# Kernel tuning notes

Measured on AMD Instinct MI355X. Metric: run time of the kernel, lower is better.

The kernel has to match this reference:

```python
import jax, jax.numpy as jnp
import numpy as np
from jax.scipy.linalg import expm

D = 512      # d_model
S = 3        # num_scales
BATCH = 256
H = 8        # attention heads
HD = D // H  # head dim


def layernorm(x, g, b, eps=1e-5):
    m = jnp.mean(x, axis=-1, keepdims=True)
    v = jnp.var(x, axis=-1, keepdims=True)
    return (x - m) / jnp.sqrt(v + eps) * g + b


def setup_inputs() -> dict:
    key = jax.random.key(0)
    ks = jax.random.split(key, 16)
    sd = 1.0 / np.sqrt(D)
    inp = {
        'x': jax.random.normal(ks[0], (BATCH, D), jnp.float32),
        'h_prev': jax.random.normal(ks[1], (BATCH, D), jnp.float32),
        'lstm_h': jax.random.normal(ks[2], (S, BATCH, D), jnp.float32) * 0.1,
        'lstm_c': jax.random.normal(ks[3], (S, BATCH, D), jnp.float32) * 0.1,
        'A': jax.random.normal(ks[4], (D, D), jnp.float32) * sd,
        'Bm': jax.random.normal(ks[5], (D, D), jnp.float32) * sd,
        'dn_w1': jax.random.normal(ks[6], (D, D), jnp.float32) * sd,
        'dn_b1': jnp.zeros((D,), jnp.float32),
        'dn_g': jnp.ones((D,), jnp.float32),
        'dn_beta': jnp.zeros((D,), jnp.float32),
        'dn_w2': jax.random.normal(ks[7], (1, D), jnp.float32) * sd,
        'dn_b2': jnp.zeros((1,), jnp.float32),
        'lstm_wih': jax.random.normal(ks[8], (S, 4 * D, D), jnp.float32) * sd,
        'lstm_whh': jax.random.normal(ks[9], (S, 4 * D, D), jnp.float32) * sd,
        'lstm_bih': jnp.zeros((S, 4 * D), jnp.float32),
        'lstm_bhh': jnp.zeros((S, 4 * D), jnp.float32),
        'decays': jnp.linspace(0.5, 0.95, S, dtype=jnp.float32),
        'attn_in_w': jax.random.normal(ks[10], (3 * D, D), jnp.float32) * sd,
        'attn_in_b': jnp.zeros((3 * D,), jnp.float32),
        'attn_out_w': jax.random.normal(ks[11], (D, D), jnp.float32) * sd,
        'attn_out_b': jnp.zeros((D,), jnp.float32),
        'proj_w': jax.random.normal(ks[12], (D, (S + 2) * D), jnp.float32) * (1.0 / np.sqrt((S + 2) * D)),
        'proj_b': jnp.zeros((D,), jnp.float32),
        'proj_g': jnp.ones((D,), jnp.float32),
        'proj_beta': jnp.zeros((D,), jnp.float32),
    }
    return inp


def reference(x, h_prev, lstm_h, lstm_c, A, Bm, dn_w1, dn_b1, dn_g, dn_beta,
              dn_w2, dn_b2, lstm_wih, lstm_whh, lstm_bih, lstm_bhh, decays,
              attn_in_w, attn_in_b, attn_out_w, attn_out_b,
              proj_w, proj_b, proj_g, proj_beta):
    # ---- delta_net: Linear -> LayerNorm -> GELU(exact) -> Linear -> Softplus ----
    h1 = layernorm(x @ dn_w1.T + dn_b1, dn_g, dn_beta)
    h1 = jax.nn.gelu(h1, approximate=False)
    delta = jax.nn.softplus(h1 @ dn_w2.T + dn_b2)           # (B, 1)

    # ---- SSM update: h_t = expm(delta*A) h_prev + delta*B x ----
    A_disc = jax.vmap(expm)(delta[:, :, None] * A)          # (B, D, D)
    h_ssm = jnp.einsum('bij,bj->bi', A_disc, h_prev) + delta * jnp.einsum('ij,bj->bi', Bm, x)

    # ---- multi-scale LSTM cells (vectorized over scales) ----
    gates = (jnp.einsum('bd,skd->sbk', x, lstm_wih)
             + jnp.einsum('sbd,skd->sbk', lstm_h, lstm_whh)
             + (lstm_bih + lstm_bhh)[:, None, :])           # (S, B, 4D)
    gi, gf, gg, go = jnp.split(gates, 4, axis=-1)
    i_g = jax.nn.sigmoid(gi)
    f_g = jax.nn.sigmoid(gf)
    g_g = jnp.tanh(gg)
    o_g = jax.nn.sigmoid(go)
    c_raw = f_g * lstm_c + i_g * g_g                        # (S, B, D)
    h_new = o_g * jnp.tanh(c_raw)                           # (S, B, D)
    dec = decays[:, None, None]
    c_new = dec * lstm_c + (1.0 - dec) * c_raw              # (S, B, D)

    # ---- fusion attention: 1 query (h_ssm), S keys/values (h_new) ----
    Wq, Wk, Wv = jnp.split(attn_in_w, 3, axis=0)
    bq, bk, bv = jnp.split(attn_in_b, 3, axis=0)
    kv = jnp.transpose(h_new, (1, 0, 2))                    # (B, S, D)
    q = (h_ssm @ Wq.T + bq).reshape(-1, 1, H, HD).transpose(0, 2, 1, 3)   # (B,H,1,HD)
    k = (kv @ Wk.T + bk).reshape(-1, S, H, HD).transpose(0, 2, 1, 3)      # (B,H,S,HD)
    v = (kv @ Wv.T + bv).reshape(-1, S, H, HD).transpose(0, 2, 1, 3)
    scores = jnp.einsum('bhqe,bhke->bhqk', q, k) / np.sqrt(HD)
    attn = jax.nn.softmax(scores, axis=-1)
    ctx = jnp.einsum('bhqk,bhke->bhqe', attn, v)            # (B,H,1,HD)
    ctx = ctx.transpose(0, 2, 1, 3).reshape(-1, D)          # (B, D)
    fused = ctx @ attn_out_w.T + attn_out_b                 # (B, D)

    # ---- output projection over concat [h_ssm, fused, h_1..h_S] ----
    combined = jnp.concatenate([h_ssm, fused] + [h_new[i] for i in range(S)], axis=-1)
    output = layernorm(combined @ proj_w.T + proj_b, proj_g, proj_beta)
    return (output, h_ssm, h_new, c_new)
```

## Files before the change

### kernel.cpp

```cpp
#include <hip/hip_runtime.h>
#include <math.h>

#define DIM 512
#define NB 256
#define KMAX 12

using bf16x8 = __attribute__((ext_vector_type(8))) short;
using f32x4  = __attribute__((ext_vector_type(4))) float;
using float4v = __attribute__((ext_vector_type(4))) float;
using ushort4v = __attribute__((ext_vector_type(4))) unsigned short;

__device__ __forceinline__ unsigned short f2b(float f) {
    union { float f; unsigned int u; } v; v.f = f;
    unsigned int r = v.u + 0x7fffu + ((v.u >> 16) & 1u);
    return (unsigned short)(r >> 16);
}
__device__ __forceinline__ float b2f(unsigned short u) {
    union { unsigned int u; float f; } v; v.u = ((unsigned int)u) << 16;
    return v.f;
}
__device__ __forceinline__ ushort4v f2b4(float4v v) {
    ushort4v o;
    o.x = f2b(v.x); o.y = f2b(v.y); o.z = f2b(v.z); o.w = f2b(v.w);
    return o;
}

__device__ __forceinline__ void block_reduce2(float& s, float& q, float* sb1, float* sb2)
{
    int tid = threadIdx.x;
    #pragma unroll
    for (int off = 32; off > 0; off >>= 1) {
        s += __shfl_down(s, off);
        q += __shfl_down(q, off);
    }
    if ((tid & 63) == 0) { sb1[tid >> 6] = s; sb2[tid >> 6] = q; }
    __syncthreads();
    s = sb1[0] + sb1[1] + sb1[2] + sb1[3];
    q = sb2[0] + sb2[1] + sb2[2] + sb2[3];
    __syncthreads();
}

struct GemmDesc {
    const unsigned short* X;
    const unsigned short* W;
    const float* bias;
    float* Cf;
    unsigned short* Cb;
    unsigned short* Ct;
    int M, N, K, ldX, ldW, ldC, tr_row0, acc;
};
struct GemmArgs { GemmDesc d[8]; };
struct LnParams {
    const float* pre; const float* g; const float* beta;
    const float* w2; const float* b2; float* delta; float* coeff;
    int lnd_y;
    const float* cin; const float* bih; const float* bhh; const float* decays;
    float* hout; float* cout; unsigned short* combb;
};

__global__ __launch_bounds__(256) void gemm_mfma(GemmArgs args, LnParams lp)
{
    __shared__ unsigned short lsA[2][8192];
    __shared__ unsigned short lsB[2][8192];
    __shared__ float sb1[4], sb2[4];

    if ((int)blockIdx.y == lp.lnd_y) {
        int b = blockIdx.x, tid = threadIdx.x;
        int i0 = tid, i1 = tid + 256;
        float x0 = lp.pre[(size_t)b * DIM + i0];
        float x1 = lp.pre[(size_t)b * DIM + i1];
        float s = x0 + x1, q = x0 * x0 + x1 * x1;
        block_reduce2(s, q, sb1, sb2);
        float mean = s * (1.f / DIM);
        float var  = q * (1.f / DIM) - mean * mean;
        float inv  = rsqrtf(var + 1e-5f);
        float y0 = (x0 - mean) * inv * lp.g[i0] + lp.beta[i0];
        float y1 = (x1 - mean) * inv * lp.g[i1] + lp.beta[i1];
        float h0 = 0.5f * y0 * (1.f + erff(y0 * 0.70710678118654752f));
        float h1 = 0.5f * y1 * (1.f + erff(y1 * 0.70710678118654752f));
        float p = h0 * lp.w2[i0] + h1 * lp.w2[i1];
        float dummy = 0.f;
        block_reduce2(p, dummy, sb1, sb2);
        if (tid == 0) {
            float z = p + lp.b2[0];
            float d = (z > 20.f) ? z : log1pf(expf(z));
            lp.delta[b] = d;
            float c = 1.f;
            lp.coeff[b] = 1.f;
            for (int k = 1; k <= KMAX; ++k) { c *= d / (float)k; lp.coeff[k * 256 + b] = c; }
        }
        return;
    }

    GemmDesc de = args.d[blockIdx.y];
    int tmm = de.M >> 6;
    int tiles = tmm * (de.N >> 6);
    int t = blockIdx.x;
    if (t >= tiles) return;
    int qc = tiles >> 3, rc = tiles & 7;
    int xcd = t & 7, li = t >> 3;
    int tt = (xcd < rc) ? (xcd * (qc + 1) + li) : (rc * (qc + 1) + (xcd - rc) * qc + li);
    int m0 = (tt % tmm) << 6;
    int n0 = (tt / tmm) << 6;

    int tid = threadIdx.x;
    int w = tid >> 6;
    int l = tid & 63;
    int nkt = de.K >> 7;

    int srow = w * 16 + (l >> 2);
    int schk = l & 3;
    const unsigned short* gA = de.X + (size_t)(m0 + srow) * de.ldX + schk * 8;
    const unsigned short* gB = de.W + (size_t)(n0 + srow) * de.ldW + schk * 8;
    unsigned short* lA = &lsA[0][(w * 64 + l) * 8];
    unsigned short* lB = &lsB[0][(w * 64 + l) * 8];

#define STAGE(bufi, kt)                                                          \
    do {                                                                         \
        for (int hh = 0; hh < 4; ++hh) {                                         \
            __builtin_amdgcn_global_load_lds(                                    \
                (const __attribute__((address_space(1))) unsigned int*)(gA + (size_t)(kt) * 128 + hh * 32), \
                (__attribute__((address_space(3))) unsigned int*)(lA + (bufi) * 8192 + hh * 2048), 16, 0, 0); \
            __builtin_amdgcn_global_load_lds(                                    \
                (const __attribute__((address_space(1))) unsigned int*)(gB + (size_t)(kt) * 128 + hh * 32), \
                (__attribute__((address_space(3))) unsigned int*)(lB + (bufi) * 8192 + hh * 2048), 16, 0, 0); \
        }                                                                        \
    } while (0)

    int mbase = (w >> 1) * 32;
    int nbase = (w & 1) * 32;

    f32x4 acc[2][2];
    #pragma unroll
    for (int i = 0; i < 2; ++i)
        #pragma unroll
        for (int j = 0; j < 2; ++j)
            acc[i][j] = (f32x4){0.f, 0.f, 0.f, 0.f};

    int kg = l >> 4;
    int fr = l & 15;
    int aslot = (mbase * 4 + fr * 4 + kg) * 8;
    int bslot = (nbase * 4 + fr * 4 + kg) * 8;

    STAGE(0, 0);

    for (int kt = 0; kt < nkt; ++kt) {
        __syncthreads();
        if (kt + 1 < nkt) STAGE((kt + 1) & 1, kt + 1);

        const unsigned short* bufA = &lsA[kt & 1][0];
        const unsigned short* bufB = &lsB[kt & 1][0];
        #pragma unroll
        for (int h = 0; h < 4; ++h) {
            bf16x8 a0 = *(const bf16x8*)(bufA + h * 2048 + aslot);
            bf16x8 a1 = *(const bf16x8*)(bufA + h * 2048 + aslot + 512);
            bf16x8 b0 = *(const bf16x8*)(bufB + h * 2048 + bslot);
            bf16x8 b1 = *(const bf16x8*)(bufB + h * 2048 + bslot + 512);
            acc[0][0] = __builtin_amdgcn_mfma_f32_16x16x32_bf16(a0, b0, acc[0][0], 0, 0, 0);
            acc[0][1] = __builtin_amdgcn_mfma_f32_16x16x32_bf16(a0, b1, acc[0][1], 0, 0, 0);
            acc[1][0] = __builtin_amdgcn_mfma_f32_16x16x32_bf16(a1, b0, acc[1][0], 0, 0, 0);
            acc[1][1] = __builtin_amdgcn_mfma_f32_16x16x32_bf16(a1, b1, acc[1][1], 0, 0, 0);
        }
    }

    if (de.acc == 3) {
        __syncthreads();
        float* tile = (float*)lsA;
        #pragma unroll
        for (int mi = 0; mi < 2; ++mi)
            #pragma unroll
            for (int ni = 0; ni < 2; ++ni) {
                int ct = nbase + ni * 16 + fr;
                #pragma unroll
                for (int r = 0; r < 4; ++r) {
                    int rt = mbase + mi * 16 + kg * 4 + r;
                    tile[rt * 65 + ct] = acc[mi][ni][r];
                }
            }
        __syncthreads();
        int s = de.tr_row0;
        int d0 = n0 >> 2;
        float dec = lp.decays[s];
        for (int cell = tid; cell < 1024; cell += 256) {
            int row = cell >> 4, dsub = cell & 15;
            int d = d0 + dsub;
            int b = m0 + row;
            float vgi = tile[row * 65 +      dsub] + lp.bih[s * 2048 +        d] + lp.bhh[s * 2048 +        d];
            float vgf = tile[row * 65 + 16 + dsub] + lp.bih[s * 2048 +  512 + d] + lp.bhh[s * 2048 +  512 + d];
            float vgg = tile[row * 65 + 32 + dsub] + lp.bih[s * 2048 + 1024 + d] + lp.bhh[s * 2048 + 1024 + d];
            float vgo = tile[row * 65 + 48 + dsub] + lp.bih[s * 2048 + 1536 + d] + lp.bhh[s * 2048 + 1536 + d];
            float cc = lp.cin[(size_t)s * 131072 + (size_t)b * 512 + d];
            float ig = 1.f / (1.f + expf(-vgi));
            float fg = 1.f / (1.f + expf(-vgf));
            float g_ = tanhf(vgg);
            float og = 1.f / (1.f + expf(-vgo));
            float craw = fg * cc + ig * g_;
            float hn = og * tanhf(craw);
            lp.hout[(size_t)s * 131072 + (size_t)b * 512 + d] = hn;
            lp.cout[(size_t)s * 131072 + (size_t)b * 512 + d] = dec * cc + (1.f - dec) * craw;
            lp.combb[(size_t)b * 2048 + 512 + s * 512 + d] = f2b(hn);
        }
        return;
    }

    #pragma unroll
    for (int mi = 0; mi < 2; ++mi) {
        #pragma unroll
        for (int ni = 0; ni < 2; ++ni) {
            int col = n0 + nbase + ni * 16 + fr;
            float bv = de.bias ? de.bias[col] : 0.f;
            #pragma unroll
            for (int r = 0; r < 4; ++r) {
                int row = m0 + mbase + mi * 16 + (l >> 4) * 4 + r;
                float v = acc[mi][ni][r] + bv;
                if (de.Cf) {
                    if (de.acc == 2)      atomicAdd(&de.Cf[(size_t)row * de.ldC + col], v);
                    else if (de.acc == 1) de.Cf[(size_t)row * de.ldC + col] += v;
                    else                  de.Cf[(size_t)row * de.ldC + col] = v;
                } else {
                    de.Cb[(size_t)row * de.ldC + col] = f2b(v);
                }
                if (de.Ct && row >= de.tr_row0)
                    de.Ct[(size_t)col * 512 + (row - de.tr_row0)] = f2b(v);
            }
        }
    }
#undef STAGE
}

#define NSEG 13
struct PrepArgs {
    const float* sA[NSEG]; const float* sB[NSEG]; unsigned short* dst[NSEG];
    int n4[NSEG], dRL4[NSEG], sRLA4[NSEG], sRLB4[NSEG], half4[NSEG], offA[NSEG], gmap[NSEG];
    const float* A; unsigned short* ATb;
    const float* W2src; unsigned short* W2dst;
    const float* projw; const float* projb; const float* aoutb; float* pbc;
};
__global__ __launch_bounds__(256) void prep_kernel(PrepArgs a)
{
    __shared__ float tile[32][33];
    int bid = blockIdx.x, tid = threadIdx.x;
    if (bid < 2048) {
        const int gstride = 2048 * 256;
        int g0 = bid * 256 + tid;
        for (int seg = 0; seg < NSEG; ++seg) {
            int n4 = a.n4[seg];
            const float* sA = a.sA[seg];
            const float* sB = a.sB[seg];
            unsigned short* d = a.dst[seg];
            int dRL4 = a.dRL4[seg], sRLA4 = a.sRLA4[seg], sRLB4 = a.sRLB4[seg];
            int half4 = a.half4[seg], offA = a.offA[seg], gm = a.gmap[seg];
            for (int i = g0; i < n4; i += gstride) {
                int r = i / dRL4, c = i - r * dRL4;
                int rs = gm ? (((r >> 4) & 3) * 512 + ((r >> 6) << 4) + (r & 15)) : r;
                const float* src = (c < half4)
                    ? sA + ((size_t)rs * sRLA4 + offA + c) * 4
                    : sB + ((size_t)rs * sRLB4 + (c - half4)) * 4;
                float4v v = *(const float4v*)src;
                *(ushort4v*)(d + (size_t)i * 4) = f2b4(v);
            }
        }
    } else if (bid < 2560) {
        int tt = bid - 2048;
        const float* src = a.A;
        unsigned short* dst = a.ATb;
        if (tt >= 256) { tt -= 256; src = a.W2src; dst = a.W2dst; }
        int bx = tt & 15, by = tt >> 4;
        int tx = tid & 31, ty = tid >> 5;
        #pragma unroll
        for (int i = 0; i < 32; i += 8)
            tile[ty + i][tx] = src[(size_t)(by * 32 + ty + i) * 512 + bx * 32 + tx];
        __syncthreads();
        #pragma unroll
        for (int i = 0; i < 32; i += 8)
            dst[(size_t)(bx * 32 + ty + i) * 512 + by * 32 + tx] = f2b(tile[tx][ty + i]);
    } else {
        int i = (bid - 2560) * 256 + tid;
        const float* pr = a.projw + (size_t)i * 2560 + 512;
        float acc = 0.f;
        for (int j = 0; j < 512; j += 4) {
            float4v w = *(const float4v*)(pr + j);
            float4v ab = *(const float4v*)(a.aoutb + j);
            acc += w.x * ab.x + w.y * ab.y + w.z * ab.z + w.w * ab.w;
        }
        a.pbc[i] = a.projb[i] + acc;
    }
}

__global__ void pointwise_fused(
    const float* __restrict__ Tm, const float* __restrict__ coeff,
    const float* __restrict__ h_prev, const float* __restrict__ delta,
    const float* __restrict__ Bx, float* __restrict__ hssm,
    unsigned short* __restrict__ combb)
{
    int idx4 = blockIdx.x * 256 + threadIdx.x;
    int base = idx4 * 4;
    int b = base >> 9, i = base & 511;
    const float* Tr = Tm + (size_t)b * (KMAX * DIM) + i;
    float4v a = *(const float4v*)(h_prev + base);
    #pragma unroll
    for (int k = 1; k <= KMAX; ++k) {
        float c = coeff[k * 256 + b];
        float4v t = *(const float4v*)(Tr + (size_t)(k - 1) * DIM);
        a.x += c * t.x; a.y += c * t.y; a.z += c * t.z; a.w += c * t.w;
    }
    float dl = delta[b];
    float4v bx = *(const float4v*)(Bx + base);
    a.x += dl * bx.x; a.y += dl * bx.y; a.z += dl * bx.z; a.w += dl * bx.w;
    *(float4v*)(hssm + base) = a;
    *(ushort4v*)(combb + (size_t)b * 2048 + i) = f2b4(a);
}

__global__ __launch_bounds__(256) void tail_kernel(
    const unsigned short* __restrict__ qb, const unsigned short* __restrict__ kvb,
    const unsigned short* __restrict__ M2b, const float* __restrict__ projA,
    const float* __restrict__ fin_g, const float* __restrict__ fin_beta,
    float* __restrict__ outp)
{
    __shared__ float ctxs[512];
    __shared__ float sb1[4], sb2[4];
    int b = blockIdx.x, tid = threadIdx.x;

    if (tid < 128) {
        int h = tid >> 4, sub = (tid & 15) * 4;
        int col = h * 64 + sub;
        ushort4v q4 = *(const ushort4v*)(qb + (size_t)b * 512 + col);
        float qf[4] = { b2f(q4.x), b2f(q4.y), b2f(q4.z), b2f(q4.w) };
        float p[3];
        ushort4v k4[3], v4[3];
        #pragma unroll
        for (int s = 0; s < 3; ++s) {
            k4[s] = *(const ushort4v*)(kvb + (size_t)s * 262144 + (size_t)b * 1024 + col);
            v4[s] = *(const ushort4v*)(kvb + (size_t)s * 262144 + (size_t)b * 1024 + 512 + col);
            p[s] = qf[0] * b2f(k4[s].x) + qf[1] * b2f(k4[s].y)
                 + qf[2] * b2f(k4[s].z) + qf[3] * b2f(k4[s].w);
        }
        #pragma unroll
        for (int off = 1; off < 16; off <<= 1) {
            p[0] += __shfl_xor(p[0], off);
            p[1] += __shfl_xor(p[1], off);
            p[2] += __shfl_xor(p[2], off);
        }
        const float scale = 0.125f;
        float p0 = p[0] * scale, p1 = p[1] * scale, p2 = p[2] * scale;
        float m = fmaxf(p0, fmaxf(p1, p2));
        float w0 = expf(p0 - m), w1 = expf(p1 - m), w2 = expf(p2 - m);
        float invs = 1.f / (w0 + w1 + w2);
        ctxs[col + 0] = (w0 * b2f(v4[0].x) + w1 * b2f(v4[1].x) + w2 * b2f(v4[2].x)) * invs;
        ctxs[col + 1] = (w0 * b2f(v4[0].y) + w1 * b2f(v4[1].y) + w2 * b2f(v4[2].y)) * invs;
        ctxs[col + 2] = (w0 * b2f(v4[0].z) + w1 * b2f(v4[1].z) + w2 * b2f(v4[2].z)) * invs;
        ctxs[col + 3] = (w0 * b2f(v4[0].w) + w1 * b2f(v4[1].w) + w2 * b2f(v4[2].w)) * invs;
    }
    __syncthreads();

    float x0 = projA[(size_t)b * 512 + tid];
    float x1 = projA[(size_t)b * 512 + tid + 256];
    {
        const unsigned short* mr0 = M2b + (size_t)tid * 512;
        const unsigned short* mr1 = M2b + (size_t)(tid + 256) * 512;
        for (int k = 0; k < 512; k += 8) {
            ushort4v a0 = *(const ushort4v*)(mr0 + k);
            ushort4v a1 = *(const ushort4v*)(mr0 + k + 4);
            ushort4v c0 = *(const ushort4v*)(mr1 + k);
            ushort4v c1 = *(const ushort4v*)(mr1 + k + 4);
            float t0 = ctxs[k+0], t1 = ctxs[k+1], t2 = ctxs[k+2], t3 = ctxs[k+3];
            float t4 = ctxs[k+4], t5 = ctxs[k+5], t6 = ctxs[k+6], t7 = ctxs[k+7];
            x0 += t0*b2f(a0.x) + t1*b2f(a0.y) + t2*b2f(a0.z) + t3*b2f(a0.w)
                + t4*b2f(a1.x) + t5*b2f(a1.y) + t6*b2f(a1.z) + t7*b2f(a1.w);
            x1 += t0*b2f(c0.x) + t1*b2f(c0.y) + t2*b2f(c0.z) + t3*b2f(c0.w)
                + t4*b2f(c1.x) + t5*b2f(c1.y) + t6*b2f(c1.z) + t7*b2f(c1.w);
        }
    }

    float s = x0 + x1, q = x0 * x0 + x1 * x1;
    block_reduce2(s, q, sb1, sb2);
    float mean = s * (1.f / DIM);
    float var  = q * (1.f / DIM) - mean * mean;
    float inv  = rsqrtf(var + 1e-5f);
    outp[(size_t)b * DIM + tid]       = (x0 - mean) * inv * fin_g[tid]       + fin_beta[tid];
    outp[(size_t)b * DIM + tid + 256] = (x1 - mean) * inv * fin_g[tid + 256] + fin_beta[tid + 256];
}

extern "C" void kernel_launch(void* const* d_in, const int* in_sizes, int n_in,
                              void* d_out, int out_size, void* d_ws, size_t ws_size,
                              hipStream_t stream)
{
    const float* x        = (const float*)d_in[0];
    const float* h_prev   = (const float*)d_in[1];
    const float* lstm_h   = (const float*)d_in[2];
    const float* lstm_c   = (const float*)d_in[3];
    const float* A        = (const float*)d_in[4];
    const float* Bm       = (const float*)d_in[5];
    const float* dn_w1    = (const float*)d_in[6];
    const float* dn_b1    = (const float*)d_in[7];
    const float* dn_g     = (const float*)d_in[8];
    const float* dn_beta  = (const float*)d_in[9];
    const float* dn_w2    = (const float*)d_in[10];
    const float* dn_b2    = (const float*)d_in[11];
    const float* wih      = (const float*)d_in[12];
    const float* whh      = (const float*)d_in[13];
    const float* bih      = (const float*)d_in[14];
    const float* bhh      = (const float*)d_in[15];
    const float* decays   = (const float*)d_in[16];
    const float* ain_w    = (const float*)d_in[17];
    const float* ain_b    = (const float*)d_in[18];
    const float* aout_w   = (const float*)d_in[19];
    const float* aout_b   = (const float*)d_in[20];
    const float* proj_w   = (const float*)d_in[21];
    const float* proj_b   = (const float*)d_in[22];
    const float* proj_g   = (const float*)d_in[23];
    const float* proj_bt  = (const float*)d_in[24];

    float* out  = (float*)d_out;
    float* hssm = out + 131072;
    float* hnew = out + 262144;
    float* cnew = out + 655360;

    unsigned short* us = (unsigned short*)d_ws;
    unsigned short* hpb     = us;
    unsigned short* ATb     = us + 131072;
    unsigned short* dn_w1b  = us + 393216;
    unsigned short* Bmb     = us + 655360;
    unsigned short* ain_wb  = us + 917504;
    unsigned short* proj_wb = us + 1703936;
    unsigned short* P2b     = us + 2752512;
    unsigned short* aout_wTb= us + 3014656;
    unsigned short* Pw      = us + 3276800;
    unsigned short* Qa      = us + 5373952;
    unsigned short* Qb      = us + 5636096;
    unsigned short* Wcat    = us + 5898240;
    unsigned short* Xcat    = us + 12189696;
    unsigned short* combb   = us + 12976128;
    unsigned short* qb      = us + 13500416;
    unsigned short* kvb     = us + 13631488;
    unsigned short* U8b     = us + 14417920;
    float* fbase  = (float*)(us + 14548992);
    float* pre1   = fbase;
    float* delta  = fbase + 131072;
    float* coeff  = fbase + 131328;
    float* Bx     = fbase + 134656;
    float* Tm     = fbase + 265728;
    float* pbc    = fbase + 1838592;
    unsigned short* M2b = (unsigned short*)(fbase + 1839616);
    float* projout = pre1;

    LnParams lpOff;
    lpOff.pre = nullptr; lpOff.g = nullptr; lpOff.beta = nullptr;
    lpOff.w2 = nullptr; lpOff.b2 = nullptr; lpOff.delta = nullptr; lpOff.coeff = nullptr;
    lpOff.lnd_y = -1;
    lpOff.cin = lstm_c; lpOff.bih = bih; lpOff.bhh = bhh; lpOff.decays = decays;
    lpOff.hout = hnew; lpOff.cout = cnew; lpOff.combb = combb;

    PrepArgs pa;
    int sidx = 0;
    auto LIN = [&](const float* s, unsigned short* d, int n4) {
        pa.sA[sidx]=s; pa.sB[sidx]=s; pa.dst[sidx]=d; pa.n4[sidx]=n4;
        pa.dRL4[sidx]=n4; pa.sRLA4[sidx]=0; pa.sRLB4[sidx]=0;
        pa.half4[sidx]=n4; pa.offA[sidx]=0; pa.gmap[sidx]=0; ++sidx;
    };
    LIN(h_prev, hpb,     32768);
    LIN(A,      Pw,      65536);
    LIN(dn_w1,  dn_w1b,  65536);
    LIN(Bm,     Bmb,     65536);
    LIN(ain_w,  ain_wb,  196608);
    pa.sA[sidx]=proj_w; pa.sB[sidx]=proj_w + 1024; pa.dst[sidx]=proj_wb; pa.n4[sidx]=262144;
    pa.dRL4[sidx]=512; pa.sRLA4[sidx]=640; pa.sRLB4[sidx]=640; pa.half4[sidx]=128; pa.offA[sidx]=0; pa.gmap[sidx]=0; ++sidx;
    pa.sA[sidx]=proj_w; pa.sB[sidx]=proj_w; pa.dst[sidx]=P2b; pa.n4[sidx]=65536;
    pa.dRL4[sidx]=128; pa.sRLA4[sidx]=640; pa.sRLB4[sidx]=640; pa.half4[sidx]=128; pa.offA[sidx]=128; pa.gmap[sidx]=0; ++sidx;
    for (int s = 0; s < 3; ++s) {
        pa.sA[sidx]=wih + (size_t)s*1048576; pa.sB[sidx]=whh + (size_t)s*1048576;
        pa.dst[sidx]=Wcat + (size_t)s*2097152; pa.n4[sidx]=524288;
        pa.dRL4[sidx]=256; pa.sRLA4[sidx]=128; pa.sRLB4[sidx]=128; pa.half4[sidx]=128; pa.offA[sidx]=0;
        pa.gmap[sidx]=1; ++sidx;
    }
    for (int s = 0; s < 3; ++s) {
        pa.sA[sidx]=x; pa.sB[sidx]=lstm_h + (size_t)s*131072;
        pa.dst[sidx]=Xcat + (size_t)s*262144; pa.n4[sidx]=65536;
        pa.dRL4[sidx]=256; pa.sRLA4[sidx]=128; pa.sRLB4[sidx]=128; pa.half4[sidx]=128; pa.offA[sidx]=0;
        pa.gmap[sidx]=0; ++sidx;
    }
    pa.A = A; pa.ATb = ATb;
    pa.W2src = aout_w; pa.W2dst = aout_wTb;
    pa.projw = proj_w; pa.projb = proj_b; pa.aoutb = aout_b; pa.pbc = pbc;
    prep_kernel<<<2562, 256, 0, stream>>>(pa);

    GemmArgs ga;
    ga.d[0] = { Xcat, dn_w1b, dn_b1, pre1, nullptr, nullptr, 256, 512, 512, 1024, 512, 512, 0, 0 };
    ga.d[1] = { Xcat, Bmb,    nullptr, Bx,  nullptr, nullptr, 256, 512, 512, 1024, 512, 512, 0, 0 };
    ga.d[2] = { Pw, ATb, nullptr, nullptr, Pw + 1*262144, Qa, 512, 512, 512, 512, 512, 512, 0, 0 };
    for (int s = 0; s < 3; ++s)
        ga.d[3 + s] = { Xcat + (size_t)s * 262144, Wcat + (size_t)s * 2097152, nullptr,
                        nullptr, nullptr, nullptr,
                        256, 2048, 1024, 1024, 1024, 2048, s, 3 };
    ga.d[6] = { P2b, aout_wTb, nullptr, nullptr, M2b, nullptr, 512, 512, 512, 512, 512, 512, 0, 0 };
    gemm_mfma<<<dim3(128, 7), 256, 0, stream>>>(ga, lpOff);

    LnParams lp1 = lpOff;
    lp1.pre = pre1; lp1.g = dn_g; lp1.beta = dn_beta; lp1.w2 = dn_w2; lp1.b2 = dn_b2;
    lp1.delta = delta; lp1.coeff = coeff; lp1.lnd_y = 1;
    ga.d[0] = { Pw, Qa, nullptr, nullptr, Pw + 2*262144, Qb, 1024, 512, 512, 512, 512, 512, 512, 0 };
    gemm_mfma<<<dim3(256, 2), 256, 0, stream>>>(ga, lp1);

    ga.d[0] = { Pw, Qb, nullptr, nullptr, Pw + 4*262144, nullptr, 2048, 512, 512, 512, 512, 512, 0, 0 };
    gemm_mfma<<<dim3(256, 1), 256, 0, stream>>>(ga, lpOff);

    ga.d[0] = { hpb, Pw, nullptr, Tm, nullptr, nullptr, 256, 4096, 512, 512, 512, 6144, 0, 0 };
    ga.d[1] = { hpb, Pw + 7*262144, nullptr, nullptr, U8b, nullptr, 256, 512, 512, 512, 512, 512, 0, 0 };
    gemm_mfma<<<dim3(256, 2), 256, 0, stream>>>(ga, lpOff);

    ga.d[0] = { U8b, Pw, nullptr, Tm + 4096, nullptr, nullptr, 256, 2048, 512, 512, 512, 6144, 0, 0 };
    gemm_mfma<<<dim3(128, 1), 256, 0, stream>>>(ga, lpOff);

    pointwise_fused<<<128, 256, 0, stream>>>(Tm, coeff, h_prev, delta, Bx, hssm, combb);

    ga.d[0] = { combb, ain_wb, ain_b, nullptr, qb, nullptr, 256, 512, 512, 2048, 512, 512, 0, 0 };
    for (int s = 0; s < 3; ++s)
        ga.d[1 + s] = { combb + 512 + (size_t)s * 512, ain_wb + 262144, ain_b + 512,
                        nullptr, kvb + (size_t)s * 262144, nullptr, 256, 1024, 512, 2048, 512, 1024, 0, 0 };
    ga.d[4] = { combb, proj_wb, pbc, projout, nullptr, nullptr, 256, 512, 2048, 2048, 2048, 512, 0, 0 };
    gemm_mfma<<<dim3(64, 5), 256, 0, stream>>>(ga, lpOff);

    tail_kernel<<<256, 256, 0, stream>>>(qb, kvb, M2b, projout,
                                         proj_g, proj_bt, out);
}
```

Before: 233.4 us.

## Interleave Taylor-series power products with matrix-power squaring chain

```diff
diff --git a/kernel.cpp b/kernel.cpp
--- a/kernel.cpp
+++ b/kernel.cpp
@@ -47,7 +47,7 @@
     float* Cf;
     unsigned short* Cb;
     unsigned short* Ct;
-    int M, N, K, ldX, ldW, ldC, tr_row0, acc;
+    int M, N, K, ldX, ldW, ldC, ldCb, tr_row0, acc;
 };
 struct GemmArgs { GemmDesc d[8]; };
 struct LnParams {
@@ -217,9 +217,9 @@
                     if (de.acc == 2)      atomicAdd(&de.Cf[(size_t)row * de.ldC + col], v);
                     else if (de.acc == 1) de.Cf[(size_t)row * de.ldC + col] += v;
                     else                  de.Cf[(size_t)row * de.ldC + col] = v;
-                } else {
-                    de.Cb[(size_t)row * de.ldC + col] = f2b(v);
                 }
+                if (de.Cb)
+                    de.Cb[(size_t)row * de.ldCb + col] = f2b(v);
                 if (de.Ct && row >= de.tr_row0)
                     de.Ct[(size_t)col * 512 + (row - de.tr_row0)] = f2b(v);
             }
@@ -433,15 +433,15 @@
     unsigned short* combb   = us + 12976128;
     unsigned short* qb      = us + 13500416;
     unsigned short* kvb     = us + 13631488;
-    unsigned short* U8b     = us + 14417920;
-    float* fbase  = (float*)(us + 14548992);
+    unsigned short* Tmb     = us + 14417920;
+    float* fbase  = (float*)(us + 14942208);
     float* pre1   = fbase;
     float* delta  = fbase + 131072;
     float* coeff  = fbase + 131328;
     float* Bx     = fbase + 134656;
     float* Tm     = fbase + 265728;
     float* pbc    = fbase + 1838592;
-    unsigned short* M2b = (unsigned short*)(fbase + 1839616);
+    unsigned short* M2b = (unsigned short*)(fbase + 1839104);
     float* projout = pre1;
 
     LnParams lpOff;
@@ -485,39 +485,46 @@
     prep_kernel<<<2562, 256, 0, stream>>>(pa);
 
     GemmArgs ga;
-    ga.d[0] = { Xcat, dn_w1b, dn_b1, pre1, nullptr, nullptr, 256, 512, 512, 1024, 512, 512, 0, 0 };
-    ga.d[1] = { Xcat, Bmb,    nullptr, Bx,  nullptr, nullptr, 256, 512, 512, 1024, 512, 512, 0, 0 };
-    ga.d[2] = { Pw, ATb, nullptr, nullptr, Pw + 1*262144, Qa, 512, 512, 512, 512, 512, 512, 0, 0 };
+    ga.d[0] = { Xcat, dn_w1b, dn_b1, pre1, nullptr, nullptr, 256, 512, 512, 1024, 512, 512, 0, 0, 0 };
+    ga.d[1] = { Xcat, Bmb,    nullptr, Bx,  nullptr, nullptr, 256, 512, 512, 1024, 512, 512, 0, 0, 0 };
+    ga.d[2] = { Pw, ATb, nullptr, nullptr, Pw + 1*262144, Qa, 512, 512, 512, 512, 512, 512, 512, 0, 0 };
     for (int s = 0; s < 3; ++s)
         ga.d[3 + s] = { Xcat + (size_t)s * 262144, Wcat + (size_t)s * 2097152, nullptr,
                         nullptr, nullptr, nullptr,
-                        256, 2048, 1024, 1024, 1024, 2048, s, 3 };
-    ga.d[6] = { P2b, aout_wTb, nullptr, nullptr, M2b, nullptr, 512, 512, 512, 512, 512, 512, 0, 0 };
-    gemm_mfma<<<dim3(128, 7), 256, 0, stream>>>(ga, lpOff);
+                        256, 2048, 1024, 1024, 1024, 2048, 0, s, 3 };
+    ga.d[6] = { P2b, aout_wTb, nullptr, nullptr, M2b, nullptr, 512, 512, 512, 512, 512, 512, 512, 0, 0 };
+    ga.d[7] = { hpb, Pw, nullptr, Tm, Tmb, nullptr, 256, 512, 512, 512, 512, 6144, 2048, 0, 0 };
+    gemm_mfma<<<dim3(128, 8), 256, 0, stream>>>(ga, lpOff);
 
     LnParams lp1 = lpOff;
     lp1.pre = pre1; lp1.g = dn_g; lp1.beta = dn_beta; lp1.w2 = dn_w2; lp1.b2 = dn_b2;
-    lp1.delta = delta; lp1.coeff = coeff; lp1.lnd_y = 1;
-    ga.d[0] = { Pw, Qa, nullptr, nullptr, Pw + 2*262144, Qb, 1024, 512, 512, 512, 512, 512, 512, 0 };
-    gemm_mfma<<<dim3(256, 2), 256, 0, stream>>>(ga, lp1);
-
-    ga.d[0] = { Pw, Qb, nullptr, nullptr, Pw + 4*262144, nullptr, 2048, 512, 512, 512, 512, 512, 0, 0 };
-    gemm_mfma<<<dim3(256, 1), 256, 0, stream>>>(ga, lpOff);
-
-    ga.d[0] = { hpb, Pw, nullptr, Tm, nullptr, nullptr, 256, 4096, 512, 512, 512, 6144, 0, 0 };
-    ga.d[1] = { hpb, Pw + 7*262144, nullptr, nullptr, U8b, nullptr, 256, 512, 512, 512, 512, 512, 0, 0 };
-    gemm_mfma<<<dim3(256, 2), 256, 0, stream>>>(ga, lpOff);
-
-    ga.d[0] = { U8b, Pw, nullptr, Tm + 4096, nullptr, nullptr, 256, 2048, 512, 512, 512, 6144, 0, 0 };
-    gemm_mfma<<<dim3(128, 1), 256, 0, stream>>>(ga, lpOff);
+    lp1.delta = delta; lp1.coeff = coeff; lp1.lnd_y = 3;
+    ga.d[0] = { Pw + 1*262144, Qa, nullptr, nullptr, Pw + 3*262144, Qb, 512, 512, 512, 512, 512, 512, 512, 0, 0 };
+    ga.d[1] = { hpb, Pw + 1*262144, nullptr, Tm + 512,  Tmb + 512,  nullptr, 256, 512, 512, 512,  512, 6144, 2048, 0, 0 };
+    ga.d[2] = { Tmb, Pw + 1*262144, nullptr, Tm + 1024, Tmb + 1024, nullptr, 256, 512, 512, 2048, 512, 6144, 2048, 0, 0 };
+    gemm_mfma<<<dim3(256, 4), 256, 0, stream>>>(ga, lp1);
+
+    ga.d[0] = { Pw + 3*262144, Qb, nullptr, nullptr, Pw + 7*262144, nullptr, 512, 512, 512, 512, 512, 512, 512, 0, 0 };
+    ga.d[1] = { hpb,        Pw + 3*262144, nullptr, Tm + 1536, Tmb + 1536, nullptr, 256, 512, 512, 512,  512, 6144, 2048, 0, 0 };
+    ga.d[2] = { Tmb,        Pw + 3*262144, nullptr, Tm + 2048, nullptr, nullptr, 256, 512, 512, 2048, 512, 6144, 0, 0, 0 };
+    ga.d[3] = { Tmb + 512,  Pw + 3*262144, nullptr, Tm + 2560, nullptr, nullptr, 256, 512, 512, 2048, 512, 6144, 0, 0, 0 };
+    ga.d[4] = { Tmb + 1024, Pw + 3*262144, nullptr, Tm + 3072, nullptr, nullptr, 256, 512, 512, 2048, 512, 6144, 0, 0, 0 };
+    gemm_mfma<<<dim3(64, 5), 256, 0, stream>>>(ga, lpOff);
+
+    ga.d[0] = { Tmb + 1536, Pw + 3*262144, nullptr, Tm + 3584, nullptr, nullptr, 256, 512, 512, 2048, 512, 6144, 0, 0, 0 };
+    ga.d[1] = { Tmb,        Pw + 7*262144, nullptr, Tm + 4096, nullptr, nullptr, 256, 512, 512, 2048, 512, 6144, 0, 0, 0 };
+    ga.d[2] = { Tmb + 512,  Pw + 7*262144, nullptr, Tm + 4608, nullptr, nullptr, 256, 512, 512, 2048, 512, 6144, 0, 0, 0 };
+    ga.d[3] = { Tmb + 1024, Pw + 7*262144, nullptr, Tm + 5120, nullptr, nullptr, 256, 512, 512, 2048, 512, 6144, 0, 0, 0 };
+    ga.d[4] = { Tmb + 1536, Pw + 7*262144, nullptr, Tm + 5632, nullptr, nullptr, 256, 512, 512, 2048, 512, 6144, 0, 0, 0 };
+    gemm_mfma<<<dim3(32, 5), 256, 0, stream>>>(ga, lpOff);
 
     pointwise_fused<<<128, 256, 0, stream>>>(Tm, coeff, h_prev, delta, Bx, hssm, combb);
 
-    ga.d[0] = { combb, ain_wb, ain_b, nullptr, qb, nullptr, 256, 512, 512, 2048, 512, 512, 0, 0 };
+    ga.d[0] = { combb, ain_wb, ain_b, nullptr, qb, nullptr, 256, 512, 512, 2048, 512, 512, 512, 0, 0 };
     for (int s = 0; s < 3; ++s)
         ga.d[1 + s] = { combb + 512 + (size_t)s * 512, ain_wb + 262144, ain_b + 512,
-                        nullptr, kvb + (size_t)s * 262144, nullptr, 256, 1024, 512, 2048, 512, 1024, 0, 0 };
-    ga.d[4] = { combb, proj_wb, pbc, projout, nullptr, nullptr, 256, 512, 2048, 2048, 2048, 512, 0, 0 };
+                        nullptr, kvb + (size_t)s * 262144, nullptr, 256, 1024, 512, 2048, 512, 1024, 1024, 0, 0 };
+    ga.d[4] = { combb, proj_wb, pbc, projout, nullptr, nullptr, 256, 512, 2048, 2048, 2048, 512, 0, 0, 0 };
     gemm_mfma<<<dim3(64, 5), 256, 0, stream>>>(ga, lpOff);
 
     tail_kernel<<<256, 256, 0, stream>>>(qb, kvb, M2b, projout,
```

Measured after the change: 225.1 us, median of 2. 3.6% less time.
